# Performance work log

Hardware: AMD Instinct MI355X
Metric: run time of the kernel (lower is better)

Reference implementation:

```python
import jax, jax.numpy as jnp
import numpy as np

HEADS = 8


def setup_inputs() -> dict:
    key = jax.random.key(0)
    k1, k2, k3, k4, k5, k6 = jax.random.split(key, 6)
    B, S, E = 2, 2048, 512
    D = E // HEADS
    return {
        "values": jax.random.normal(k1, (B, S, E), dtype=jnp.float32),
        "keys": jax.random.normal(k2, (B, S, E), dtype=jnp.float32),
        "queries": jax.random.normal(k3, (B, S, E), dtype=jnp.float32),
        "mask": jax.random.randint(k4, (B, 1, 1, S), 0, 2, dtype=jnp.int32),
        "W_v": jax.random.normal(k5, (D, D), dtype=jnp.float32) * (1.0 / np.sqrt(D)),
        "W_o": jax.random.normal(k6, (E, E), dtype=jnp.float32) * (1.0 / np.sqrt(E)),
        "b_o": jnp.zeros((E,), dtype=jnp.float32),
    }


def reference(values, keys, queries, mask, W_v, W_o, b_o):
    B, S, E = queries.shape
    H = HEADS
    D = E // H
    # reshape to (b, s, h, d) and apply the SAME W_v linear to v, k, q
    # (faithful to the original, which calls self.values on all three)
    v = jnp.einsum('bshd,ed->bshe', values.reshape(B, -1, H, D), W_v)
    k = jnp.einsum('bshd,ed->bshe', keys.reshape(B, -1, H, D), W_v)
    q = jnp.einsum('bshd,ed->bshe', queries.reshape(B, -1, H, D), W_v)
    # unscaled attention scores (original has no 1/sqrt(d))
    energy = jnp.einsum('bqhd,bkhd->bhqk', q, k)  # (b, h, q, k)
    energy = jnp.where(mask == 0, -jnp.inf, energy)
    attn = jax.nn.softmax(energy, axis=3)
    out = jnp.einsum('bhqk,bkhd->bqhd', attn, v)  # (b, q, h, d)
    out = out.reshape(B, S, E)
    return out @ W_o.T + b_o
```

## Files before the change

kernel.cpp:

```cpp
#include <hip/hip_runtime.h>


#define B_ 2
#define S_ 2048
#define E_ 512
#define H_ 8
#define D_ 64

#define LOG2E 1.4426950408889634f
#define KEEP_BIAS (-92.332483f)

typedef unsigned short ushort_t;
typedef __attribute__((ext_vector_type(8))) short short8;
typedef __attribute__((ext_vector_type(8))) _Float16 half8;
typedef __attribute__((ext_vector_type(4))) float f32x4;

__device__ __forceinline__ ushort_t f2bs(float x) {
    union { float f; unsigned int u; } a; a.f = x;
    unsigned int u = a.u;
    u += 0x7fffu + ((u >> 16) & 1u);
    return (ushort_t)(u >> 16);
}
__device__ __forceinline__ ushort_t f2hs(float x) {
    _Float16 h = (_Float16)x;
    ushort_t u; __builtin_memcpy(&u, &h, 2);
    return u;
}

__global__ void __launch_bounds__(256) proj_mfma(
    const float* __restrict__ quer, const float* __restrict__ keys,
    const float* __restrict__ vals, const float* __restrict__ Wv,
    const float* __restrict__ Wo,
    ushort_t* __restrict__ qf, ushort_t* __restrict__ kf,
    ushort_t* __restrict__ vt, ushort_t* __restrict__ Wob)
{
    __shared__ ushort_t As[3][64 * 72];
    __shared__ ushort_t Bs[64 * 72];
    const int bx = blockIdx.x;
    const int t = threadIdx.x;

    if (blockIdx.y == 1) {
        if (bx < 128) {
            int g = (bx * 256 + t) * 8;
            float4 f0 = *(const float4*)(Wo + g);
            float4 f1 = *(const float4*)(Wo + g + 4);
            ushort_t tmp[8] = {f2bs(f0.x), f2bs(f0.y), f2bs(f0.z), f2bs(f0.w),
                               f2bs(f1.x), f2bs(f1.y), f2bs(f1.z), f2bs(f1.w)};
            *(uint4*)&Wob[g] = *(uint4*)tmp;
        }
        return;
    }

    const int st = bx & 31, bh = bx >> 5;
    const int b = bh >> 3, h = bh & 7;
    const int s0 = st * 64;

    {
        int e = t >> 2, dg = (t & 3) * 16;
        const float4* g = (const float4*)(Wv + e * 64 + dg);
        ushort_t tmp[16];
        #pragma unroll
        for (int q = 0; q < 4; ++q) {
            float4 f = g[q];
            tmp[q * 4 + 0] = f2hs(f.x); tmp[q * 4 + 1] = f2hs(f.y);
            tmp[q * 4 + 2] = f2hs(f.z); tmp[q * 4 + 3] = f2hs(f.w);
        }
        *(uint4*)&Bs[e * 72 + dg]     = *(uint4*)tmp;
        *(uint4*)&Bs[e * 72 + dg + 8] = *(uint4*)(tmp + 8);
    }
    {
        int row = t >> 2, cg = (t & 3) * 16;
        const size_t off = ((size_t)b * S_ + s0 + row) * 512 + h * 64 + cg;
        const float* srcs[3] = {quer, keys, vals};
        #pragma unroll
        for (int tt = 0; tt < 3; ++tt) {
            const float4* g = (const float4*)(srcs[tt] + off);
            ushort_t tmp[16];
            #pragma unroll
            for (int q = 0; q < 4; ++q) {
                float4 f = g[q];
                tmp[q * 4 + 0] = f2hs(f.x); tmp[q * 4 + 1] = f2hs(f.y);
                tmp[q * 4 + 2] = f2hs(f.z); tmp[q * 4 + 3] = f2hs(f.w);
            }
            *(uint4*)&As[tt][row * 72 + cg]     = *(uint4*)tmp;
            *(uint4*)&As[tt][row * 72 + cg + 8] = *(uint4*)(tmp + 8);
        }
    }
    __syncthreads();

    const int w = t >> 6, lm = t & 15, quad = (t >> 4) & 3;

    #pragma unroll
    for (int tens = 0; tens < 3; ++tens) {
        f32x4 acc[4];
        #pragma unroll
        for (int nt = 0; nt < 4; ++nt) acc[nt] = (f32x4){0.f, 0.f, 0.f, 0.f};

        __builtin_amdgcn_s_setprio(1);
        #pragma unroll
        for (int kk = 0; kk < 2; ++kk) {
            half8 a = *(const half8*)&As[tens][(w * 16 + lm) * 72 + kk * 32 + quad * 8];
            #pragma unroll
            for (int nt = 0; nt < 4; ++nt) {
                half8 bb = *(const half8*)&Bs[(nt * 16 + lm) * 72 + kk * 32 + quad * 8];
                acc[nt] = __builtin_amdgcn_mfma_f32_16x16x32_f16(a, bb, acc[nt], 0, 0, 0);
            }
        }
        __builtin_amdgcn_s_setprio(0);

        if (tens < 2) {
            ushort_t* dst = tens == 0 ? qf : kf;
            const float sc = tens == 0 ? LOG2E : 1.0f;
            #pragma unroll
            for (int nt = 0; nt < 4; ++nt) {
                #pragma unroll
                for (int r = 0; r < 4; ++r) {
                    size_t addr = ((size_t)bh * S_ + s0 + w * 16 + quad * 4 + r) * 64 + nt * 16 + lm;
                    dst[addr] = f2hs(acc[nt][r] * sc);
                }
            }
        } else {
            #pragma unroll
            for (int nt = 0; nt < 4; ++nt) {
                unsigned int p0 = (unsigned int)f2bs(acc[nt][0]) | ((unsigned int)f2bs(acc[nt][1]) << 16);
                unsigned int p1 = (unsigned int)f2bs(acc[nt][2]) | ((unsigned int)f2bs(acc[nt][3]) << 16);
                uint2 pk; pk.x = p0; pk.y = p1;
                size_t addr = ((size_t)bh * 64 + nt * 16 + lm) * S_ + s0 + w * 16 + quad * 4;
                *(uint2*)&vt[addr] = pk;
            }
        }
    }
}

__global__ void __launch_bounds__(512, 4) attn_mfma(
    const ushort_t* __restrict__ qf, const ushort_t* __restrict__ kf,
    const ushort_t* __restrict__ vt, const int* __restrict__ mask,
    ushort_t* __restrict__ ctx)
{
    __shared__ ushort_t Ks[2][64 * 72];
    __shared__ ushort_t Vt[2][64 * 72];
    __shared__ ushort_t Ps[8][16 * 40];
    __shared__ float    mb[2][64];

    const int bx = blockIdx.x;
    const int qt = bx & 31;
    const int bh = bx >> 5;
    const int b  = bh >> 3;
    const int t  = threadIdx.x;
    const int w  = t >> 6;
    const int wq = w & 3;
    const int ws = w >> 2;
    const int lm = t & 15, quad = (t >> 4) & 3;
    const int q0 = qt * 64;

    const int srow = t >> 3;
    const int scg  = (t & 7) * 8;
    const size_t kgbase = ((size_t)bh * S_ + srow) * 64 + scg;
    const size_t vgbase = ((size_t)bh * 64 + srow) * S_ + scg;

    half8 aq[2];
    {
        size_t qrow = ((size_t)bh * S_ + q0 + wq * 16 + lm) * 64 + quad * 8;
        aq[0] = *(const half8*)&qf[qrow];
        aq[1] = *(const half8*)&qf[qrow + 32];
    }
    short8 ones;
    #pragma unroll
    for (int j = 0; j < 8; ++j) ones[j] = (short)0x3F80;

    f32x4 acc[4];
    #pragma unroll
    for (int nt = 0; nt < 4; ++nt) acc[nt] = (f32x4){0.f, 0.f, 0.f, 0.f};
    f32x4 acc_l = (f32x4){0.f, 0.f, 0.f, 0.f};

    {
        *(uint4*)&Ks[0][srow * 72 + scg] = *(const uint4*)&kf[kgbase];
        *(uint4*)&Vt[0][srow * 72 + scg] = *(const uint4*)&vt[vgbase];
        if (t < 64) mb[0][t] = mask[b * S_ + t] ? KEEP_BIAS : -1e30f;
    }
    __syncthreads();

    for (int is = 0; is < 32; ++is) {
        const int p = is & 1;
        const bool pf = is < 31;

        uint4 pk0, pv0; int mnx = 0;
        if (pf) {
            pk0 = *(const uint4*)&kf[kgbase + (size_t)(is + 1) * 4096];
            pv0 = *(const uint4*)&vt[vgbase + (size_t)(is + 1) * 64];
            if (t < 64) mnx = mask[b * S_ + (is + 1) * 64 + t];
        }

        const ushort_t* Kc = Ks[p];
        const ushort_t* Vc = Vt[p];

        #pragma unroll
        for (int ntk = 0; ntk < 2; ++ntk) {
            f32x4 s = *(const f32x4*)&mb[p][ws * 32 + ntk * 16 + quad * 4];
            __builtin_amdgcn_s_setprio(1);
            #pragma unroll
            for (int kk = 0; kk < 2; ++kk) {
                half8 ak = *(const half8*)&Kc[(ws * 32 + ntk * 16 + lm) * 72 + kk * 32 + quad * 8];
                s = __builtin_amdgcn_mfma_f32_16x16x32_f16(ak, aq[kk], s, 0, 0, 0);
            }
            __builtin_amdgcn_s_setprio(0);
            float p0 = __builtin_amdgcn_exp2f(s[0]);
            float p1 = __builtin_amdgcn_exp2f(s[1]);
            float p2 = __builtin_amdgcn_exp2f(s[2]);
            float p3 = __builtin_amdgcn_exp2f(s[3]);
            uint2 pkd;
            pkd.x = (unsigned int)f2bs(p0) | ((unsigned int)f2bs(p1) << 16);
            pkd.y = (unsigned int)f2bs(p2) | ((unsigned int)f2bs(p3) << 16);
            *(uint2*)&Ps[w][lm * 40 + ntk * 16 + quad * 4] = pkd;
        }

        __builtin_amdgcn_s_setprio(1);
        {
            short8 ap = *(const short8*)&Ps[w][lm * 40 + quad * 8];
            #pragma unroll
            for (int nt = 0; nt < 4; ++nt) {
                short8 bv = *(const short8*)&Vc[(nt * 16 + lm) * 72 + ws * 32 + quad * 8];
                acc[nt] = __builtin_amdgcn_mfma_f32_16x16x32_bf16(ap, bv, acc[nt], 0, 0, 0);
            }
            acc_l = __builtin_amdgcn_mfma_f32_16x16x32_bf16(ap, ones, acc_l, 0, 0, 0);
        }
        __builtin_amdgcn_s_setprio(0);

        if (pf) {
            *(uint4*)&Ks[p ^ 1][srow * 72 + scg] = pk0;
            *(uint4*)&Vt[p ^ 1][srow * 72 + scg] = pv0;
            if (t < 64) mb[p ^ 1][t] = mnx ? KEEP_BIAS : -1e30f;
        }
        __syncthreads();
    }

    float* cfO = (float*)Ks;
    float* cfL = (float*)Vt;
    const int lane = t & 63;
    if (ws == 1) {
        const int bO = (wq * 64 + lane) * 17;
        const int bL = (wq * 64 + lane) * 5;
        #pragma unroll
        for (int nt = 0; nt < 4; ++nt)
            #pragma unroll
            for (int r = 0; r < 4; ++r) cfO[bO + nt * 4 + r] = acc[nt][r];
        #pragma unroll
        for (int r = 0; r < 4; ++r) cfL[bL + r] = acc_l[r];
    }
    __syncthreads();
    if (ws == 0) {
        const int bO = (wq * 64 + lane) * 17;
        const int bL = (wq * 64 + lane) * 5;
        const int h = bh & 7;
        #pragma unroll
        for (int r = 0; r < 4; ++r) {
            float l = acc_l[r] + cfL[bL + r];
            float inv = 1.f / l;
            int s = q0 + wq * 16 + quad * 4 + r;
            #pragma unroll
            for (int nt = 0; nt < 4; ++nt) {
                float o = acc[nt][r] + cfO[bO + nt * 4 + r];
                ctx[((size_t)b * S_ + s) * E_ + h * D_ + nt * 16 + lm] = f2bs(o * inv);
            }
        }
    }
}

__global__ void __launch_bounds__(512, 4) outproj_mfma(
    const ushort_t* __restrict__ ctx, const ushort_t* __restrict__ Wob,
    const float* __restrict__ bo, float* __restrict__ out)
{
    __shared__ ushort_t sm[4][64 * 72];
    const int m0 = blockIdx.x * 64, n0 = blockIdx.y * 64;
    const int t = threadIdx.x;
    const int w = t >> 6, wq = w & 3, wk = w >> 2;
    const int lm = t & 15, quad = (t >> 4) & 3;
    const int srow = t >> 3, scg = (t & 7) * 8;

    const size_t abase = (size_t)(m0 + srow) * E_ + scg;
    const size_t bbase = (size_t)(n0 + srow) * E_ + scg;

    f32x4 acc[4];
    #pragma unroll
    for (int nt = 0; nt < 4; ++nt) acc[nt] = (f32x4){0.f, 0.f, 0.f, 0.f};

    *(uint4*)&sm[0][srow * 72 + scg] = *(const uint4*)&ctx[abase];
    *(uint4*)&sm[1][srow * 72 + scg] = *(const uint4*)&ctx[abase + 256];
    *(uint4*)&sm[2][srow * 72 + scg] = *(const uint4*)&Wob[bbase];
    *(uint4*)&sm[3][srow * 72 + scg] = *(const uint4*)&Wob[bbase + 256];
    __syncthreads();

    const ushort_t* Ac = sm[wk];
    const ushort_t* Bc = sm[2 + wk];

    for (int is = 0; is < 4; ++is) {
        const bool pf = is < 3;
        uint4 pa0, pa1, pb0, pb1;
        if (pf) {
            pa0 = *(const uint4*)&ctx[abase + (size_t)(is + 1) * 64];
            pa1 = *(const uint4*)&ctx[abase + 256 + (size_t)(is + 1) * 64];
            pb0 = *(const uint4*)&Wob[bbase + (size_t)(is + 1) * 64];
            pb1 = *(const uint4*)&Wob[bbase + 256 + (size_t)(is + 1) * 64];
        }

        __builtin_amdgcn_s_setprio(1);
        #pragma unroll
        for (int kk = 0; kk < 2; ++kk) {
            short8 a = *(const short8*)&Ac[(wq * 16 + lm) * 72 + kk * 32 + quad * 8];
            #pragma unroll
            for (int nt = 0; nt < 4; ++nt) {
                short8 bb = *(const short8*)&Bc[(nt * 16 + lm) * 72 + kk * 32 + quad * 8];
                acc[nt] = __builtin_amdgcn_mfma_f32_16x16x32_bf16(a, bb, acc[nt], 0, 0, 0);
            }
        }
        __builtin_amdgcn_s_setprio(0);

        __syncthreads();
        if (pf) {
            *(uint4*)&sm[0][srow * 72 + scg] = pa0;
            *(uint4*)&sm[1][srow * 72 + scg] = pa1;
            *(uint4*)&sm[2][srow * 72 + scg] = pb0;
            *(uint4*)&sm[3][srow * 72 + scg] = pb1;
            __syncthreads();
        }
    }

    float* cf = (float*)sm;
    const int lane = t & 63;
    if (wk == 1) {
        const int base = (wq * 64 + lane) * 18;
        #pragma unroll
        for (int nt = 0; nt < 4; ++nt) {
            #pragma unroll
            for (int r = 0; r < 4; r += 2) {
                float2 v2; v2.x = acc[nt][r]; v2.y = acc[nt][r + 1];
                *(float2*)&cf[base + nt * 4 + r] = v2;
            }
        }
    }
    __syncthreads();
    if (wk == 0) {
        const int base = (wq * 64 + lane) * 18;
        #pragma unroll
        for (int nt = 0; nt < 4; ++nt) {
            float bias = bo[n0 + nt * 16 + lm];
            #pragma unroll
            for (int r = 0; r < 4; ++r) {
                int m = m0 + wq * 16 + quad * 4 + r;
                out[(size_t)m * E_ + n0 + nt * 16 + lm] =
                    acc[nt][r] + cf[base + nt * 4 + r] + bias;
            }
        }
    }
}

extern "C" void kernel_launch(void* const* d_in, const int* in_sizes, int n_in,
                              void* d_out, int out_size, void* d_ws, size_t ws_size,
                              hipStream_t stream) {
    const float* vals = (const float*)d_in[0];
    const float* keys = (const float*)d_in[1];
    const float* quer = (const float*)d_in[2];
    const int*   mask = (const int*)d_in[3];
    const float* Wv   = (const float*)d_in[4];
    const float* Wo   = (const float*)d_in[5];
    const float* bo   = (const float*)d_in[6];
    float* out = (float*)d_out;

    const size_t N = (size_t)B_ * H_ * S_ * D_;
    ushort_t* ws  = (ushort_t*)d_ws;
    ushort_t* qf  = ws;
    ushort_t* kf  = ws + N;
    ushort_t* vt  = ws + 2 * N;
    ushort_t* ctx = ws + 3 * N;
    ushort_t* Wob = ws + 4 * N;

    proj_mfma<<<dim3(B_ * H_ * (S_ / 64), 2), 256, 0, stream>>>(
        quer, keys, vals, Wv, Wo, qf, kf, vt, Wob);
    attn_mfma<<<B_ * H_ * (S_ / 64), 512, 0, stream>>>(qf, kf, vt, mask, ctx);
    outproj_mfma<<<dim3((B_ * S_) / 64, E_ / 64), 512, 0, stream>>>(ctx, Wob, bo, out);
}
```

Before: 126.7 us.

## Process 128-key chunks per iteration with each wave-half owning a 64-key tile

Reorganizes the attention loop so each iteration loads two 64-key K/V tiles, and each half of the waves processes its own full tile in two 32-key phases instead of sharing one tile split by wave. This halves the number of loop iterations, and the launch bounds change to six waves per EU. The double buffer now holds both tiles of one iteration rather than ping-ponging, so an extra barrier is needed before the next tiles are stored. Prefetch registers double, which may conflict with the higher occupancy target.

```diff
diff --git a/kernel.cpp b/kernel.cpp
--- a/kernel.cpp
+++ b/kernel.cpp
@@ -132,7 +132,7 @@
     }
 }
 
-__global__ void __launch_bounds__(512, 4) attn_mfma(
+__global__ void __launch_bounds__(512, 6) attn_mfma(
     const ushort_t* __restrict__ qf, const ushort_t* __restrict__ kf,
     const ushort_t* __restrict__ vt, const int* __restrict__ mask,
     ushort_t* __restrict__ ctx)
@@ -175,63 +175,75 @@
 
     {
         *(uint4*)&Ks[0][srow * 72 + scg] = *(const uint4*)&kf[kgbase];
+        *(uint4*)&Ks[1][srow * 72 + scg] = *(const uint4*)&kf[kgbase + 4096];
         *(uint4*)&Vt[0][srow * 72 + scg] = *(const uint4*)&vt[vgbase];
-        if (t < 64) mb[0][t] = mask[b * S_ + t] ? KEEP_BIAS : -1e30f;
-    }
-    __syncthreads();
-
-    for (int is = 0; is < 32; ++is) {
-        const int p = is & 1;
-        const bool pf = is < 31;
-
-        uint4 pk0, pv0; int mnx = 0;
+        *(uint4*)&Vt[1][srow * 72 + scg] = *(const uint4*)&vt[vgbase + 64];
+        if (t < 128) mb[t >> 6][t & 63] = mask[b * S_ + t] ? KEEP_BIAS : -1e30f;
+    }
+    __syncthreads();
+
+    for (int is = 0; is < S_ / 128; ++is) {
+        const bool pf = (is + 1) < (S_ / 128);
+
+        uint4 pk0, pk1, pv0, pv1; int mnx = 0;
         if (pf) {
-            pk0 = *(const uint4*)&kf[kgbase + (size_t)(is + 1) * 4096];
-            pv0 = *(const uint4*)&vt[vgbase + (size_t)(is + 1) * 64];
-            if (t < 64) mnx = mask[b * S_ + (is + 1) * 64 + t];
-        }
-
-        const ushort_t* Kc = Ks[p];
-        const ushort_t* Vc = Vt[p];
-
-        #pragma unroll
-        for (int ntk = 0; ntk < 2; ++ntk) {
-            f32x4 s = *(const f32x4*)&mb[p][ws * 32 + ntk * 16 + quad * 4];
+            size_t ko = kgbase + (size_t)(2 * (is + 1)) * 4096;
+            pk0 = *(const uint4*)&kf[ko];
+            pk1 = *(const uint4*)&kf[ko + 4096];
+            size_t vo = vgbase + (size_t)(2 * (is + 1)) * 64;
+            pv0 = *(const uint4*)&vt[vo];
+            pv1 = *(const uint4*)&vt[vo + 64];
+            if (t < 128) mnx = mask[b * S_ + (2 * (is + 1)) * 64 + t];
+        }
+
+        const ushort_t* Kc = Ks[ws];
+        const ushort_t* Vc = Vt[ws];
+
+        #pragma unroll
+        for (int ph = 0; ph < 2; ++ph) {
+            #pragma unroll
+            for (int nn = 0; nn < 2; ++nn) {
+                const int nt = ph * 2 + nn;
+                f32x4 s = *(const f32x4*)&mb[ws][nt * 16 + quad * 4];
+                __builtin_amdgcn_s_setprio(1);
+                #pragma unroll
+                for (int kk = 0; kk < 2; ++kk) {
+                    half8 ak = *(const half8*)&Kc[(nt * 16 + lm) * 72 + kk * 32 + quad * 8];
+                    s = __builtin_amdgcn_mfma_f32_16x16x32_f16(ak, aq[kk], s, 0, 0, 0);
+                }
+                __builtin_amdgcn_s_setprio(0);
+                float p0 = __builtin_amdgcn_exp2f(s[0]);
+                float p1 = __builtin_amdgcn_exp2f(s[1]);
+                float p2 = __builtin_amdgcn_exp2f(s[2]);
+                float p3 = __builtin_amdgcn_exp2f(s[3]);
+                uint2 pkd;
+                pkd.x = (unsigned int)f2bs(p0) | ((unsigned int)f2bs(p1) << 16);
+                pkd.y = (unsigned int)f2bs(p2) | ((unsigned int)f2bs(p3) << 16);
+                *(uint2*)&Ps[w][lm * 40 + nn * 16 + quad * 4] = pkd;
+            }
+
             __builtin_amdgcn_s_setprio(1);
-            #pragma unroll
-            for (int kk = 0; kk < 2; ++kk) {
-                half8 ak = *(const half8*)&Kc[(ws * 32 + ntk * 16 + lm) * 72 + kk * 32 + quad * 8];
-                s = __builtin_amdgcn_mfma_f32_16x16x32_f16(ak, aq[kk], s, 0, 0, 0);
+            {
+                short8 ap = *(const short8*)&Ps[w][lm * 40 + quad * 8];
+                #pragma unroll
+                for (int nt = 0; nt < 4; ++nt) {
+                    short8 bv = *(const short8*)&Vc[(nt * 16 + lm) * 72 + ph * 32 + quad * 8];
+                    acc[nt] = __builtin_amdgcn_mfma_f32_16x16x32_bf16(ap, bv, acc[nt], 0, 0, 0);
+                }
+                acc_l = __builtin_amdgcn_mfma_f32_16x16x32_bf16(ap, ones, acc_l, 0, 0, 0);
             }
             __builtin_amdgcn_s_setprio(0);
-            float p0 = __builtin_amdgcn_exp2f(s[0]);
-            float p1 = __builtin_amdgcn_exp2f(s[1]);
-            float p2 = __builtin_amdgcn_exp2f(s[2]);
-            float p3 = __builtin_amdgcn_exp2f(s[3]);
-            uint2 pkd;
-            pkd.x = (unsigned int)f2bs(p0) | ((unsigned int)f2bs(p1) << 16);
-            pkd.y = (unsigned int)f2bs(p2) | ((unsigned int)f2bs(p3) << 16);
-            *(uint2*)&Ps[w][lm * 40 + ntk * 16 + quad * 4] = pkd;
-        }
-
-        __builtin_amdgcn_s_setprio(1);
-        {
-            short8 ap = *(const short8*)&Ps[w][lm * 40 + quad * 8];
-            #pragma unroll
-            for (int nt = 0; nt < 4; ++nt) {
-                short8 bv = *(const short8*)&Vc[(nt * 16 + lm) * 72 + ws * 32 + quad * 8];
-                acc[nt] = __builtin_amdgcn_mfma_f32_16x16x32_bf16(ap, bv, acc[nt], 0, 0, 0);
-            }
-            acc_l = __builtin_amdgcn_mfma_f32_16x16x32_bf16(ap, ones, acc_l, 0, 0, 0);
-        }
-        __builtin_amdgcn_s_setprio(0);
-
+        }
+
+        __syncthreads();
         if (pf) {
-            *(uint4*)&Ks[p ^ 1][srow * 72 + scg] = pk0;
-            *(uint4*)&Vt[p ^ 1][srow * 72 + scg] = pv0;
-            if (t < 64) mb[p ^ 1][t] = mnx ? KEEP_BIAS : -1e30f;
-        }
-        __syncthreads();
+            *(uint4*)&Ks[0][srow * 72 + scg] = pk0;
+            *(uint4*)&Ks[1][srow * 72 + scg] = pk1;
+            *(uint4*)&Vt[0][srow * 72 + scg] = pv0;
+            *(uint4*)&Vt[1][srow * 72 + scg] = pv1;
+            if (t < 128) mb[t >> 6][t & 63] = mnx ? KEEP_BIAS : -1e30f;
+            __syncthreads();
+        }
     }
 
     float* cfO = (float*)Ks;
```

Result: no change. 126.4 us (-0.2%).
